# Optimization experiments

Hardware: AMD Instinct MI355X
Metric: run time of the kernel (lower is better)

Reference implementation:

```python
import jax, jax.numpy as jnp
import numpy as np

N = 50000      # nodes
E = 1200000    # edges (before self loops)
IN = 128       # in_channels
HID = 32       # hidden_channels
HEADS = 2
HC = HID * HEADS  # 64, per-layer output channels
OUT = 40       # classes
NEG_SLOPE = 0.2
BN_EPS = 1e-5


def setup_inputs() -> dict:
    key = jax.random.key(0)
    ks = jax.random.split(key, 20)
    def nrm(k, shape, scale=0.1):
        return jax.random.normal(k, shape, dtype=jnp.float32) * scale
    return {
        "x": jax.random.normal(ks[0], (N, IN), dtype=jnp.float32),
        "edge_index": jax.random.randint(ks[1], (2, E), 0, N),
        "W1": nrm(ks[2], (IN, HC)),
        "a_src1": nrm(ks[3], (HEADS, HID)),
        "a_dst1": nrm(ks[4], (HEADS, HID)),
        "b1": nrm(ks[5], (HC,)),
        "bn_gamma": 1.0 + nrm(ks[6], (HC,)),
        "bn_beta": nrm(ks[7], (HC,)),
        "bn_mean": nrm(ks[8], (HC,)),
        "bn_var": jax.random.uniform(ks[9], (HC,), minval=0.5, maxval=1.5),
        "W2": nrm(ks[10], (HC, HC)),
        "a_src2": nrm(ks[11], (HEADS, HID)),
        "a_dst2": nrm(ks[12], (HEADS, HID)),
        "b2": nrm(ks[13], (HC,)),
        "Wf": nrm(ks[14], (HC, OUT)),
        "bf": nrm(ks[15], (OUT,)),
    }


def _gat_conv(x, src, dst, W, a_s, a_d, b):
    # x: [N, F_in] -> h: [N, H, C]
    h = (x @ W).reshape(N, HEADS, HID)
    alpha_src = jnp.einsum("nhc,hc->nh", h, a_s)  # [N, H]
    alpha_dst = jnp.einsum("nhc,hc->nh", h, a_d)  # [N, H]
    e = alpha_src[src] + alpha_dst[dst]            # [E, H]
    e = jnp.where(e > 0, e, NEG_SLOPE * e)         # leaky_relu(0.2)
    # scatter softmax over edges grouped by dst node
    m = jax.ops.segment_max(e, dst, num_segments=N)
    m = jnp.where(jnp.isfinite(m), m, 0.0)         # isolated nodes -> -inf fill
    ee = jnp.exp(e - m[dst])
    denom = jax.ops.segment_sum(ee, dst, num_segments=N)
    alpha = ee / (denom[dst] + 1e-16)              # [E, H]
    # gather src features, weight by attention, scatter-add to dst
    out = jax.ops.segment_sum(h[src] * alpha[:, :, None], dst, num_segments=N)
    return out.reshape(N, HC) + b                  # concat heads + bias


def reference(x, edge_index, W1, a_src1, a_dst1, b1, bn_gamma, bn_beta,
              bn_mean, bn_var, W2, a_src2, a_dst2, b2, Wf, bf):
    # PyG GATConv adds self loops by default
    loop = jnp.arange(N, dtype=edge_index.dtype)
    src = jnp.concatenate([edge_index[0], loop])
    dst = jnp.concatenate([edge_index[1], loop])

    x1 = _gat_conv(x, src, dst, W1, a_src1, a_dst1, b1)
    x1 = (x1 - bn_mean) / jnp.sqrt(bn_var + BN_EPS) * bn_gamma + bn_beta  # BN eval
    x1 = jax.nn.elu(x1)
    # dropout is identity in eval mode
    x2 = _gat_conv(x1, src, dst, W2, a_src2, a_dst2, b2)
    jk = jnp.maximum(x1, x2)  # JumpingKnowledge 'max'
    logits = jk @ Wf + bf
    return jax.nn.log_softmax(logits, axis=1)
```

## Files before the change

### kernel.cpp

```cpp
#include <hip/hip_runtime.h>
#include <hip/hip_bf16.h>
#include <math.h>

#define N_NODES 50000
#define E_EDGES 1200000
#define E_TOT   (E_EDGES + N_NODES)
#define NEG_SLOPE 0.2f
#define BN_EPS 1e-5f
#define P_PART 196
#define B1 256
#define NSCAN (P_PART * B1)

__device__ __forceinline__ int rl_i(int v, int l) {
    return __builtin_amdgcn_readlane(v, l);
}
__device__ __forceinline__ float rl_f(float v, int l) {
    return __uint_as_float(__builtin_amdgcn_readlane(__float_as_uint(v), l));
}
__device__ __forceinline__ unsigned bf16_bits(float f) {
    unsigned u = __float_as_uint(f);
    return (u + 0x7FFFu + ((u >> 16) & 1u)) >> 16;
}

__global__ void hist_kernel(const int* __restrict__ edst, unsigned* __restrict__ Ghist) {
    __shared__ unsigned hist[P_PART];
    for (int i = threadIdx.x; i < P_PART; i += 256) hist[i] = 0;
    __syncthreads();
    const int chunk = (E_TOT + B1 - 1) / B1;
    const int beg = blockIdx.x * chunk;
    const int end = min(beg + chunk, E_TOT);
    for (int i = beg + threadIdx.x; i < end; i += 256) {
        int d = (i < E_EDGES) ? edst[i] : (i - E_EDGES);
        atomicAdd(&hist[d >> 8], 1u);
    }
    __syncthreads();
    for (int p = threadIdx.x; p < P_PART; p += 256)
        Ghist[p * B1 + blockIdx.x] = hist[p];
}

__global__ void scan2_kernel(const unsigned* __restrict__ Ghist, unsigned* __restrict__ Goff) {
    __shared__ unsigned lds[1024];
    const int t = threadIdx.x;
    const int C = (NSCAN + 1023) / 1024;
    const int beg = t * C;
    const int end = min(beg + C, NSCAN);
    unsigned sum = 0;
    for (int i = beg; i < end; ++i) sum += Ghist[i];
    lds[t] = sum;
    __syncthreads();
    for (int off = 1; off < 1024; off <<= 1) {
        unsigned x = (t >= off) ? lds[t - off] : 0;
        __syncthreads();
        lds[t] += x;
        __syncthreads();
    }
    unsigned run = (t == 0) ? 0 : lds[t - 1];
    for (int i = beg; i < end; ++i) { Goff[i] = run; run += Ghist[i]; }
}

__global__ void partbase_kernel(const unsigned* __restrict__ Goff,
                                int* __restrict__ partbase, int* __restrict__ ptr) {
    int p = threadIdx.x;
    if (p < P_PART) partbase[p] = (int)Goff[p * B1];
    if (p == P_PART) partbase[P_PART] = E_TOT;
    if (p == 0) ptr[N_NODES] = E_TOT;
}

__global__ void scat2_kernel(const int* __restrict__ esrc, const int* __restrict__ edst,
                             const unsigned* __restrict__ Goff, unsigned* __restrict__ Gpart) {
    __shared__ unsigned cur[P_PART];
    for (int p = threadIdx.x; p < P_PART; p += 256) cur[p] = Goff[p * B1 + blockIdx.x];
    __syncthreads();
    const int chunk = (E_TOT + B1 - 1) / B1;
    const int beg = blockIdx.x * chunk;
    const int end = min(beg + chunk, E_TOT);
    for (int i = beg + threadIdx.x; i < end; i += 256) {
        int s = (i < E_EDGES) ? esrc[i] : (i - E_EDGES);
        int d = (i < E_EDGES) ? edst[i] : (i - E_EDGES);
        unsigned slot = atomicAdd(&cur[d >> 8], 1u);
        Gpart[slot] = ((unsigned)(d & 255) << 16) | (unsigned)s;
    }
}

__global__ void csr_kernel(const int* __restrict__ partbase, const unsigned* __restrict__ Gpart,
                           int* __restrict__ ptr, unsigned short* __restrict__ csr,
                           unsigned short* __restrict__ dl16) {
    __shared__ unsigned deg[256];
    __shared__ unsigned scn[256];
    const int p = blockIdx.x;
    const int t = threadIdx.x;
    const int base = partbase[p];
    const int cnt = partbase[p + 1] - base;
    deg[t] = 0;
    __syncthreads();
    for (int i = t; i < cnt; i += 256)
        atomicAdd(&deg[Gpart[base + i] >> 16], 1u);
    __syncthreads();
    unsigned v = deg[t];
    scn[t] = v;
    __syncthreads();
    for (int o = 1; o < 256; o <<= 1) {
        unsigned x = (t >= o) ? scn[t - o] : 0;
        __syncthreads();
        scn[t] += x;
        __syncthreads();
    }
    unsigned excl = scn[t] - v;
    int node = p * 256 + t;
    if (node < N_NODES) ptr[node] = base + (int)excl;
    __syncthreads();
    deg[t] = excl;
    __syncthreads();
    for (int i = t; i < cnt; i += 256) {
        unsigned rec = Gpart[base + i];
        unsigned dl = rec >> 16;
        unsigned slot = atomicAdd(&deg[dl], 1u);
        csr[base + slot]  = (unsigned short)(rec & 0xFFFFu);
        dl16[base + slot] = (unsigned short)dl;
    }
}

__global__ void ew_kernel(const int* __restrict__ partbase,
                          const unsigned short* __restrict__ csr,
                          const unsigned short* __restrict__ dl16,
                          const float2* __restrict__ asrc,
                          const float2* __restrict__ adst,
                          uint2* __restrict__ wrec,
                          float2* __restrict__ denom) {
    __shared__ float2 sad[256];
    __shared__ float sden[512];
    const int p = blockIdx.x, t = threadIdx.x;
    if (t < 256) {
        int node = p * 256 + t;
        sad[t] = (node < N_NODES) ? adst[node] : make_float2(0.f, 0.f);
    }
    if (t < 512) sden[t] = 0.f;
    __syncthreads();
    const int base = partbase[p];
    const int cnt = partbase[p + 1] - base;
    for (int i = t; i < cnt; i += 1024) {
        int s  = (int)csr[base + i];
        int dl = (int)dl16[base + i];
        float2 a = asrc[s];
        float2 b = sad[dl];
        float e0 = a.x + b.x; e0 = e0 > 0.f ? e0 : NEG_SLOPE * e0;
        float e1 = a.y + b.y; e1 = e1 > 0.f ? e1 : NEG_SLOPE * e1;
        float w0 = __expf(e0), w1 = __expf(e1);
        atomicAdd(&sden[dl * 2 + 0], w0);
        atomicAdd(&sden[dl * 2 + 1], w1);
        wrec[base + i] = make_uint2((unsigned)s | (bf16_bits(w0) << 16), bf16_bits(w1));
    }
    __syncthreads();
    if (t < 256) {
        int node = p * 256 + t;
        if (node < N_NODES) denom[node] = make_float2(sden[t * 2], sden[t * 2 + 1]);
    }
}

template<int K>
__global__ void lin_att_kernel(const float* __restrict__ x,
                               const float* __restrict__ W,
                               const float* __restrict__ a_s,
                               const float* __restrict__ a_d,
                               __hip_bfloat16* __restrict__ h,
                               float* __restrict__ asrc,
                               float* __restrict__ adst,
                               int n) {
    __shared__ float sW[K * 64];
    const int tid = threadIdx.x, lane = tid & 63;
    for (int i = tid; i < K * 64; i += 256) sW[i] = W[i];
    __syncthreads();
    const float a_sv = a_s[lane];
    const float a_dv = a_d[lane];
    const int wid = blockIdx.x * 4 + (tid >> 6);
    const int nwaves = gridDim.x * 4;
    for (int node = wid; node < n; node += nwaves) {
        float xr[K / 64];
        #pragma unroll
        for (int p = 0; p < K / 64; ++p) xr[p] = x[node * K + p * 64 + lane];
        float acc = 0.f;
        #pragma unroll
        for (int p = 0; p < K / 64; ++p) {
            #pragma unroll
            for (int k = 0; k < 64; ++k) {
                float xk = rl_f(xr[p], k);
                acc = fmaf(xk, sW[(p * 64 + k) * 64 + lane], acc);
            }
        }
        h[node * 64 + lane] = __float2bfloat16(acc);
        float ps = acc * a_sv, pd = acc * a_dv;
        #pragma unroll
        for (int m = 1; m < 32; m <<= 1) {
            ps += __shfl_xor(ps, m, 64);
            pd += __shfl_xor(pd, m, 64);
        }
        if ((lane & 31) == 0) {
            asrc[node * 2 + (lane >> 5)] = ps;
            adst[node * 2 + (lane >> 5)] = pd;
        }
    }
}

template<bool BN, bool FINAL>
__global__ void gat_agg_kernel(const int* __restrict__ ptr,
                               const uint2* __restrict__ wrec,
                               const float2* __restrict__ denom,
                               const __hip_bfloat16* __restrict__ h,
                               const float* __restrict__ bias,
                               const float* __restrict__ gamma, const float* __restrict__ beta,
                               const float* __restrict__ mean, const float* __restrict__ var,
                               float* __restrict__ out,
                               const float* __restrict__ x1, const float* __restrict__ Wf,
                               const float* __restrict__ bf, float* __restrict__ out40) {
    __shared__ float sWf[FINAL ? 64 * 40 : 1];
    if constexpr (FINAL) {
        for (int i = threadIdx.x; i < 64 * 40; i += 256) sWf[i] = Wf[i];
        __syncthreads();
    }
    int node = blockIdx.x * 4 + (threadIdx.x >> 6);
    if (node >= N_NODES) return;
    const int lane = threadIdx.x & 63;
    const int half = lane & 31;
    const bool lo = (lane < 32);
    float2 dn = denom[node];
    const float den = lo ? dn.x : dn.y;
    float acc = 0.f;
    const int beg = ptr[node], end = ptr[node + 1];

#define EDGE(J) {                                                            \
        unsigned rx = (unsigned)rl_i((int)rec.x, (J));                       \
        unsigned ry = (unsigned)rl_i((int)rec.y, (J));                       \
        const __hip_bfloat16* hp = h + (size_t)(rx & 0xFFFFu) * 64u;         \
        float wv = __uint_as_float(lo ? (rx & 0xFFFF0000u) : (ry << 16));    \
        acc = fmaf(wv, __bfloat162float(hp[lane]), acc); }

    for (int base = beg; base < end; base += 32) {
        const int cnt = min(32, end - base);
        uint2 rec = make_uint2(0u, 0u);
        if (half < cnt) rec = wrec[base + half];
        int j = 0;
        for (; j + 8 <= cnt; j += 8) {
            EDGE(j) EDGE(j + 1) EDGE(j + 2) EDGE(j + 3)
            EDGE(j + 4) EDGE(j + 5) EDGE(j + 6) EDGE(j + 7)
        }
        for (; j < cnt; ++j) { EDGE(j) }
    }
#undef EDGE

    float v = acc / (den + 1e-16f) + bias[lane];
    if constexpr (BN) {
        v = (v - mean[lane]) * rsqrtf(var[lane] + BN_EPS) * gamma[lane] + beta[lane];
        v = v > 0.f ? v : (__expf(v) - 1.f);
    }
    if constexpr (FINAL) {
        float jk = fmaxf(x1[node * 64 + lane], v);
        const int o = (lane < 40) ? lane : 0;
        float dot = 0.f;
        #pragma unroll
        for (int c = 0; c < 64; ++c) {
            float jv = rl_f(jk, c);
            dot = fmaf(jv, sWf[c * 40 + o], dot);
        }
        float logit = (lane < 40) ? (dot + bf[o]) : -INFINITY;
        float mx = logit;
        #pragma unroll
        for (int mm = 1; mm < 64; mm <<= 1) mx = fmaxf(mx, __shfl_xor(mx, mm, 64));
        float ex = (lane < 40) ? __expf(logit - mx) : 0.f;
        float sum = ex;
        #pragma unroll
        for (int mm = 1; mm < 64; mm <<= 1) sum += __shfl_xor(sum, mm, 64);
        if (lane < 40) out40[node * 40 + lane] = logit - mx - logf(sum);
    } else {
        out[node * 64 + lane] = v;
    }
}

extern "C" void kernel_launch(void* const* d_in, const int* in_sizes, int n_in,
                              void* d_out, int out_size, void* d_ws, size_t ws_size,
                              hipStream_t stream) {
    const float* x     = (const float*)d_in[0];
    const int*   ei    = (const int*)d_in[1];
    const float* W1    = (const float*)d_in[2];
    const float* as1   = (const float*)d_in[3];
    const float* ad1   = (const float*)d_in[4];
    const float* b1    = (const float*)d_in[5];
    const float* gamma = (const float*)d_in[6];
    const float* beta  = (const float*)d_in[7];
    const float* mean  = (const float*)d_in[8];
    const float* var   = (const float*)d_in[9];
    const float* W2    = (const float*)d_in[10];
    const float* as2   = (const float*)d_in[11];
    const float* ad2   = (const float*)d_in[12];
    const float* b2    = (const float*)d_in[13];
    const float* Wf    = (const float*)d_in[14];
    const float* bf    = (const float*)d_in[15];
    float* out = (float*)d_out;
    const int* esrc = ei;
    const int* edst = ei + E_EDGES;

    char* ws = (char*)d_ws;
    size_t off = 0;
    auto alloc = [&](size_t bytes) {
        char* p = ws + off;
        off += (bytes + 255) & ~(size_t)255;
        return p;
    };
    unsigned* Ghist = (unsigned*)alloc((size_t)NSCAN * 4);
    unsigned* Goff  = (unsigned*)alloc((size_t)NSCAN * 4);
    int* partbase   = (int*)alloc((size_t)(P_PART + 1) * 4);
    unsigned* Gpart = (unsigned*)alloc((size_t)E_TOT * 4);
    int* ptr              = (int*)alloc((size_t)(N_NODES + 1) * 4);
    unsigned short* csr   = (unsigned short*)alloc((size_t)E_TOT * 2);
    unsigned short* dl16  = (unsigned short*)alloc((size_t)E_TOT * 2);
    uint2* wrec           = (uint2*)alloc((size_t)E_TOT * 8);
    float2* denom         = (float2*)alloc((size_t)N_NODES * 8);
    __hip_bfloat16* hbuf  = (__hip_bfloat16*)alloc((size_t)N_NODES * 64 * 2);
    float* x1buf = (float*)alloc((size_t)N_NODES * 64 * 4);
    float* asrc  = (float*)alloc((size_t)N_NODES * 2 * 4);
    float* adst  = (float*)alloc((size_t)N_NODES * 2 * 4);
    (void)ws_size; (void)in_sizes; (void)n_in; (void)out_size;

    const int NB = (N_NODES + 3) / 4;

    hist_kernel<<<B1, 256, 0, stream>>>(edst, Ghist);
    scan2_kernel<<<1, 1024, 0, stream>>>(Ghist, Goff);
    partbase_kernel<<<1, 256, 0, stream>>>(Goff, partbase, ptr);
    scat2_kernel<<<B1, 256, 0, stream>>>(esrc, edst, Goff, Gpart);
    csr_kernel<<<P_PART, 256, 0, stream>>>(partbase, Gpart, ptr, csr, dl16);

    lin_att_kernel<128><<<2048, 256, 0, stream>>>(x, W1, as1, ad1, hbuf, asrc, adst, N_NODES);
    ew_kernel<<<P_PART, 1024, 0, stream>>>(partbase, csr, dl16,
        (const float2*)asrc, (const float2*)adst, wrec, denom);
    gat_agg_kernel<true, false><<<NB, 256, 0, stream>>>(ptr, wrec, denom, hbuf,
        b1, gamma, beta, mean, var, x1buf, nullptr, nullptr, nullptr, nullptr);

    lin_att_kernel<64><<<2048, 256, 0, stream>>>(x1buf, W2, as2, ad2, hbuf, asrc, adst, N_NODES);
    ew_kernel<<<P_PART, 1024, 0, stream>>>(partbase, csr, dl16,
        (const float2*)asrc, (const float2*)adst, wrec, denom);
    gat_agg_kernel<false, true><<<NB, 256, 0, stream>>>(ptr, wrec, denom, hbuf,
        b2, nullptr, nullptr, nullptr, nullptr, nullptr, x1buf, Wf, bf, out);
}
```

Before: 290.5 us.

## Register-tile the linear+attention kernel over 64-node shared-memory tiles

```diff
diff --git a/kernel.cpp b/kernel.cpp
--- a/kernel.cpp
+++ b/kernel.cpp
@@ -158,45 +158,68 @@
 }
 
 template<int K>
-__global__ void lin_att_kernel(const float* __restrict__ x,
-                               const float* __restrict__ W,
-                               const float* __restrict__ a_s,
-                               const float* __restrict__ a_d,
-                               __hip_bfloat16* __restrict__ h,
-                               float* __restrict__ asrc,
-                               float* __restrict__ adst,
-                               int n) {
+__global__ __launch_bounds__(256) void lin_att_kernel(
+        const float* __restrict__ x, const float* __restrict__ W,
+        const float* __restrict__ a_s, const float* __restrict__ a_d,
+        __hip_bfloat16* __restrict__ h, float* __restrict__ asrc,
+        float* __restrict__ adst) {
+    __shared__ float sx[64 * (K + 1)];
     __shared__ float sW[K * 64];
-    const int tid = threadIdx.x, lane = tid & 63;
+    const int tid = threadIdx.x;
     for (int i = tid; i < K * 64; i += 256) sW[i] = W[i];
-    __syncthreads();
-    const float a_sv = a_s[lane];
-    const float a_dv = a_d[lane];
-    const int wid = blockIdx.x * 4 + (tid >> 6);
-    const int nwaves = gridDim.x * 4;
-    for (int node = wid; node < n; node += nwaves) {
-        float xr[K / 64];
+    const int ng = tid >> 4;
+    const int cg = tid & 15;
+    const int c0 = cg * 4;
+    const float4 asv = *(const float4*)&a_s[c0];
+    const float4 adv = *(const float4*)&a_d[c0];
+    const int ntiles = (N_NODES + 63) / 64;
+    for (int tile = blockIdx.x; tile < ntiles; tile += gridDim.x) {
+        const int nbase = tile * 64;
+        __syncthreads();
+        for (int i = tid; i < 64 * K; i += 256) {
+            int n = i / K, k = i - n * K;
+            int node = nbase + n;
+            sx[n * (K + 1) + k] = (node < N_NODES) ? x[(size_t)node * K + k] : 0.f;
+        }
+        __syncthreads();
+        float acc[4][4] = {};
+        #pragma unroll 4
+        for (int k = 0; k < K; ++k) {
+            float4 wv = *(const float4*)&sW[k * 64 + c0];
+            #pragma unroll
+            for (int j = 0; j < 4; ++j) {
+                float xv = sx[(ng * 4 + j) * (K + 1) + k];
+                acc[j][0] = fmaf(xv, wv.x, acc[j][0]);
+                acc[j][1] = fmaf(xv, wv.y, acc[j][1]);
+                acc[j][2] = fmaf(xv, wv.z, acc[j][2]);
+                acc[j][3] = fmaf(xv, wv.w, acc[j][3]);
+            }
+        }
         #pragma unroll
-        for (int p = 0; p < K / 64; ++p) xr[p] = x[node * K + p * 64 + lane];
-        float acc = 0.f;
-        #pragma unroll
-        for (int p = 0; p < K / 64; ++p) {
+        for (int j = 0; j < 4; ++j) {
+            int node = nbase + ng * 4 + j;
+            float ps = acc[j][0] * asv.x + acc[j][1] * asv.y +
+                       acc[j][2] * asv.z + acc[j][3] * asv.w;
+            float pd = acc[j][0] * adv.x + acc[j][1] * adv.y +
+                       acc[j][2] * adv.z + acc[j][3] * adv.w;
             #pragma unroll
-            for (int k = 0; k < 64; ++k) {
-                float xk = rl_f(xr[p], k);
-                acc = fmaf(xk, sW[(p * 64 + k) * 64 + lane], acc);
+            for (int o = 1; o < 8; o <<= 1) {
+                ps += __shfl_xor(ps, o, 64);
+                pd += __shfl_xor(pd, o, 64);
             }
-        }
-        h[node * 64 + lane] = __float2bfloat16(acc);
-        float ps = acc * a_sv, pd = acc * a_dv;
-        #pragma unroll
-        for (int m = 1; m < 32; m <<= 1) {
-            ps += __shfl_xor(ps, m, 64);
-            pd += __shfl_xor(pd, m, 64);
-        }
-        if ((lane & 31) == 0) {
-            asrc[node * 2 + (lane >> 5)] = ps;
-            adst[node * 2 + (lane >> 5)] = pd;
+            if (node < N_NODES) {
+                ushort4 pk;
+                pk.x = (unsigned short)bf16_bits(acc[j][0]);
+                pk.y = (unsigned short)bf16_bits(acc[j][1]);
+                pk.z = (unsigned short)bf16_bits(acc[j][2]);
+                pk.w = (unsigned short)bf16_bits(acc[j][3]);
+                *(ushort4*)&h[(size_t)node * 64 + c0] = pk;
+                if ((cg & 7) == 0) {
+                    int head = cg >> 3;
+                    asrc[node * 2 + head] = ps;
+                    adst[node * 2 + head] = pd;
+                }
+            }
         }
     }
 }
@@ -321,6 +344,7 @@
     (void)ws_size; (void)in_sizes; (void)n_in; (void)out_size;
 
     const int NB = (N_NODES + 3) / 4;
+    const int GT = (N_NODES + 63) / 64;
 
     hist_kernel<<<B1, 256, 0, stream>>>(edst, Ghist);
     scan2_kernel<<<1, 1024, 0, stream>>>(Ghist, Goff);
@@ -328,13 +352,13 @@
     scat2_kernel<<<B1, 256, 0, stream>>>(esrc, edst, Goff, Gpart);
     csr_kernel<<<P_PART, 256, 0, stream>>>(partbase, Gpart, ptr, csr, dl16);
 
-    lin_att_kernel<128><<<2048, 256, 0, stream>>>(x, W1, as1, ad1, hbuf, asrc, adst, N_NODES);
+    lin_att_kernel<128><<<GT, 256, 0, stream>>>(x, W1, as1, ad1, hbuf, asrc, adst);
     ew_kernel<<<P_PART, 1024, 0, stream>>>(partbase, csr, dl16,
         (const float2*)asrc, (const float2*)adst, wrec, denom);
     gat_agg_kernel<true, false><<<NB, 256, 0, stream>>>(ptr, wrec, denom, hbuf,
         b1, gamma, beta, mean, var, x1buf, nullptr, nullptr, nullptr, nullptr);
 
-    lin_att_kernel<64><<<2048, 256, 0, stream>>>(x1buf, W2, as2, ad2, hbuf, asrc, adst, N_NODES);
+    lin_att_kernel<64><<<GT, 256, 0, stream>>>(x1buf, W2, as2, ad2, hbuf, asrc, adst);
     ew_kernel<<<P_PART, 1024, 0, stream>>>(partbase, csr, dl16,
         (const float2*)asrc, (const float2*)adst, wrec, denom);
     gat_agg_kernel<false, true><<<NB, 256, 0, stream>>>(ptr, wrec, denom, hbuf,
```

New measurement: 269.4 us. 1.08x faster.
